# Performance work log

Measured on AMD Instinct MI355X. Metric: run time of the kernel, lower is better.

## Reference

```python
import jax, jax.numpy as jnp
import numpy as np

N_USERS, N_ITEMS, N_ENT = 2500, 3000, 2500
N = N_USERS + N_ITEMS + N_ENT
D, NREL, L, K, NH = 128, 32, 2, 16, 2
NE = 256_000
F_MOVIE, F_USER = 768, 512
GATE_T = 0.5


def _lin(x, w, b):
    return x @ w + b


def setup_inputs() -> dict:
    key = jax.random.key(0)
    ks = iter(jax.random.split(key, 64))
    def rn(shape, s=0.05):
        return jax.random.normal(next(ks), shape, jnp.float32) * s
    def zb():
        return jnp.zeros((D,), jnp.float32)
    inp = dict(
        user_w=rn((N_USERS, D), 0.1), item_w=rn((N_ITEMS, D), 0.1),
        ent_w=rn((N_ENT, D), 0.1), rel_w=rn((NREL, D), 0.1),
        mfeat=rn((N_ITEMS, F_MOVIE), 1.0), ufeat=rn((N_USERS, F_USER), 1.0),
        me_w1=rn((F_MOVIE, D)), me_b1=zb(), me_w2=rn((D, D)), me_b2=zb(),
        ue_w1=rn((F_USER, D)), ue_b1=zb(), ue_w2=rn((D, D)), ue_b2=zb(),
        cm_qw=rn((D, D)), cm_qb=zb(), cm_kw=rn((D, D)), cm_kb=zb(),
        cm_vw=rn((D, D)), cm_vb=zb(), cm_ow=rn((D, D)), cm_ob=zb(),
        mg_w=rn((2 * D, D)), mg_b=zb(), ug_w=rn((2 * D, D)), ug_b=zb(),
        gnn_qw=rn((L, D, D)), gnn_qb=jnp.zeros((L, D), jnp.float32),
        gnn_kw=rn((L, D, D)), gnn_kb=jnp.zeros((L, D), jnp.float32),
        gnn_vw=rn((L, D, D)), gnn_vb=jnp.zeros((L, D), jnp.float32),
        la_w=rn(((L + 1) * D, D)), la_b=zb(),
        adj_data=jax.random.uniform(next(ks), (NE,), jnp.float32, 1e-3, 1.0),
        adj_row=jax.random.randint(next(ks), (NE,), 0, N),
        adj_col=jax.random.randint(next(ks), (NE,), 0, N),
    )
    return inp


def _forward(user_w, item_w, ent_w, rel_w, mfeat, ufeat,
             me_w1, me_b1, me_w2, me_b2, ue_w1, ue_b1, ue_w2, ue_b2,
             cm_qw, cm_qb, cm_kw, cm_kb, cm_vw, cm_vb, cm_ow, cm_ob,
             mg_w, mg_b, ug_w, ug_b,
             gnn_qw, gnn_qb, gnn_kw, gnn_kb, gnn_vw, gnn_vb,
             la_w, la_b, adj_data, adj_row, adj_col):
    hd = D // NH
    # --- modality encoders (dropout is inference-mode identity) ---
    mm_item = jax.nn.relu(_lin(jax.nn.relu(_lin(mfeat, me_w1, me_b1)), me_w2, me_b2))
    mm_user = jax.nn.relu(_lin(jax.nn.relu(_lin(ufeat, ue_w1, ue_b1)), ue_w2, ue_b2))
    # --- MultiHeadCrossModalAttention(mm_item, mm_item): 2 modalities ---
    x = jnp.stack([mm_item, mm_item], axis=1)                     # [B, 2, D]
    B, M = x.shape[0], x.shape[1]
    q = _lin(x, cm_qw, cm_qb).reshape(B, M, NH, hd).transpose(0, 2, 1, 3)
    k = _lin(x, cm_kw, cm_kb).reshape(B, M, NH, hd).transpose(0, 2, 1, 3)
    v = _lin(x, cm_vw, cm_vb).reshape(B, M, NH, hd).transpose(0, 2, 1, 3)
    attn = jax.nn.softmax(jnp.einsum('bhmd,bhnd->bhmn', q, k) / jnp.sqrt(jnp.float32(hd)), axis=-1)
    ao = jnp.einsum('bhmn,bhnd->bhmd', attn, v).transpose(0, 2, 1, 3).reshape(B, M, D)
    mm_item = _lin(ao, cm_ow, cm_ob).sum(axis=1)                  # [B, D]
    # --- gated fusion (NOTE: double sigmoid, faithful to source) ---
    mg = jax.nn.sigmoid(jax.nn.sigmoid(_lin(jnp.concatenate([item_w, mm_item], axis=-1), mg_w, mg_b)) / GATE_T)
    fused_item = mg * item_w + (1.0 - mg) * mm_item + 0.1 * item_w
    ug = jax.nn.sigmoid(jax.nn.sigmoid(_lin(jnp.concatenate([user_w, mm_user], axis=-1), ug_w, ug_b)) / GATE_T)
    fused_user = ug * user_w + (1.0 - ug) * mm_user + 0.1 * user_w
    # --- GNN propagation with SparseKnowledgeAttention ---
    emb = jnp.concatenate([fused_user, fused_item, ent_w], axis=0)  # [N, D]
    rel_mean = rel_w.mean(axis=0)                                  # [D]
    embs = [emb]
    for l in range(L):
        e = embs[-1]
        # sparse adj @ e via gather + segment_sum
        side = jax.ops.segment_sum(adj_data[:, None] * e[adj_col], adj_row, num_segments=N)
        qn = _lin(e, gnn_qw[l], gnn_qb[l])
        kn = _lin(side * rel_mean[None, :], gnn_kw[l], gnn_kb[l])
        scores = (qn @ kn.T) / jnp.sqrt(jnp.float32(D))            # [N, N]
        tv, ti = jax.lax.top_k(scores, K)                          # [N, K]
        w = jax.nn.softmax(tv, axis=-1)
        vn = _lin(side, gnn_vw[l], gnn_vb[l])
        agg = jnp.einsum('nk,nkd->nd', w, vn[ti])                  # gather + weighted sum
        embs.append(jax.nn.relu(agg))
    final = _lin(jnp.concatenate(embs, axis=-1), la_w, la_b)       # layer_agg on stacked layers
    def _norm(z):
        return z / jnp.maximum(jnp.linalg.norm(z, axis=1, keepdims=True), 1e-12)
    return (_norm(final[:N_USERS]),
            _norm(final[N_USERS:N_USERS + N_ITEMS]),
            item_w, mm_item)


def reference(user_w, item_w, ent_w, rel_w, mfeat, ufeat,
              me_w1, me_b1, me_w2, me_b2, ue_w1, ue_b1, ue_w2, ue_b2,
              cm_qw, cm_qb, cm_kw, cm_kb, cm_vw, cm_vb, cm_ow, cm_ob,
              mg_w, mg_b, ug_w, ug_b,
              gnn_qw, gnn_qb, gnn_kw, gnn_kb, gnn_vw, gnn_vb,
              la_w, la_b, adj_data, adj_row, adj_col):
    return _forward(user_w, item_w, ent_w, rel_w, mfeat, ufeat,
                    me_w1, me_b1, me_w2, me_b2, ue_w1, ue_b1, ue_w2, ue_b2,
                    cm_qw, cm_qb, cm_kw, cm_kb, cm_vw, cm_vb, cm_ow, cm_ob,
                    mg_w, mg_b, ug_w, ug_b,
                    gnn_qw, gnn_qb, gnn_kw, gnn_kb, gnn_vw, gnn_vb,
                    la_w, la_b, adj_data, adj_row, adj_col)
```

## Files before the change

kernel.cpp:

```cpp
#include <hip/hip_runtime.h>
#include <hip/hip_bf16.h>
#include <math.h>

#define N_USERS 2500
#define N_ITEMS 3000
#define N_ENT   2500
#define NTOT    8000
#define D       128
#define NEDGE   256000
#define NSLICE  8
#define NMAT    12

typedef unsigned short u16;
typedef unsigned int u32;
typedef unsigned long long u64;
typedef __attribute__((ext_vector_type(8))) short short8;
typedef __attribute__((ext_vector_type(4))) float f32x4;

static __device__ __forceinline__ u16 bf16bits(float x) {
  __hip_bfloat16 h = __float2bfloat16(x);
  return *reinterpret_cast<u16*>(&h);
}

struct WsplitArgs {
  const float* w[NMAT];
  int useks[NMAT];
  int K[NMAT];
  int cum[NMAT + 1];
  int ofs[NMAT];
};

__global__ void k_wsplit_all(WsplitArgs a, const float* __restrict__ relmean,
                             u16* __restrict__ arena) {
  const int e = blockIdx.x * 256 + threadIdx.x;
  if (e >= a.cum[NMAT]) return;
  int i = 0;
  while (e >= a.cum[i + 1]) ++i;
  const int local = e - a.cum[i];
  const int k = local >> 7, j = local & 127;
  const int K = a.K[i];
  float x = a.w[i][(size_t)k * 128 + j];
  if (a.useks[i]) x *= relmean[k];
  const __hip_bfloat16 h1 = __float2bfloat16(x);
  const float r1 = x - __bfloat162float(h1);
  const __hip_bfloat16 h2 = __float2bfloat16(r1);
  const float r2 = r1 - __bfloat162float(h2);
  const __hip_bfloat16 h3 = __float2bfloat16(r2);
  u16* __restrict__ base = arena + a.ofs[i] + (size_t)j * K + k;
  base[0]                 = *(const u16*)&h1;
  base[(size_t)128 * K]   = *(const u16*)&h2;
  base[(size_t)256 * K * 1 + (size_t)0] = base[(size_t)256 * K];
  base[(size_t)256 * K]   = *(const u16*)&h3;
}

__global__ __launch_bounds__(256) void k_gemm3(const float* __restrict__ A,
                                               const u16* __restrict__ wsg,
                                               const float* __restrict__ b,
                                               float* __restrict__ out,
                                               u16* __restrict__ ob,
                                               int M, int K, int mode) {
  const int tid  = threadIdx.x;
  const int lane = tid & 63;
  const int wave = tid >> 6;
  const int rbase = blockIdx.x * 64 + wave * 16;
  const int colL = lane & 15;
  const int kofs = (lane >> 4) * 8;

  f32x4 acc[8];
#pragma unroll
  for (int ct = 0; ct < 8; ++ct) acc[ct] = (f32x4){0.f, 0.f, 0.f, 0.f};

  const int arow = (rbase + colL < M) ? (rbase + colL) : (M - 1);
  const float* __restrict__ arp = A + (size_t)arow * K;

  for (int k0 = 0; k0 < K; k0 += 32) {
    const float4 f0 = *(const float4*)(arp + k0 + kofs);
    const float4 f1 = *(const float4*)(arp + k0 + kofs + 4);
    float av[8] = {f0.x, f0.y, f0.z, f0.w, f1.x, f1.y, f1.z, f1.w};
    short8 a1, a2, a3;
#pragma unroll
    for (int e = 0; e < 8; ++e) {
      const float x = av[e];
      const __hip_bfloat16 h1 = __float2bfloat16(x);
      const float r1 = x - __bfloat162float(h1);
      const __hip_bfloat16 h2 = __float2bfloat16(r1);
      const float r2 = r1 - __bfloat162float(h2);
      const __hip_bfloat16 h3 = __float2bfloat16(r2);
      a1[e] = *(const short*)&h1;
      a2[e] = *(const short*)&h2;
      a3[e] = *(const short*)&h3;
    }
#pragma unroll
    for (int ct = 0; ct < 8; ++ct) {
      const int j = ct * 16 + colL;
      const u16* wp = wsg + (size_t)j * K + k0 + kofs;
      const short8 b1 = *(const short8*)wp;
      const short8 b2 = *(const short8*)(wp + (size_t)128 * K);
      const short8 b3 = *(const short8*)(wp + (size_t)256 * K);
      acc[ct] = __builtin_amdgcn_mfma_f32_16x16x32_bf16(a1, b1, acc[ct], 0, 0, 0);
      acc[ct] = __builtin_amdgcn_mfma_f32_16x16x32_bf16(a1, b2, acc[ct], 0, 0, 0);
      acc[ct] = __builtin_amdgcn_mfma_f32_16x16x32_bf16(a2, b1, acc[ct], 0, 0, 0);
      acc[ct] = __builtin_amdgcn_mfma_f32_16x16x32_bf16(a2, b2, acc[ct], 0, 0, 0);
      acc[ct] = __builtin_amdgcn_mfma_f32_16x16x32_bf16(a1, b3, acc[ct], 0, 0, 0);
      acc[ct] = __builtin_amdgcn_mfma_f32_16x16x32_bf16(a3, b1, acc[ct], 0, 0, 0);
    }
  }

#pragma unroll
  for (int ct = 0; ct < 8; ++ct) {
    const int j = ct * 16 + colL;
    const float bj = b[j];
#pragma unroll
    for (int r = 0; r < 4; ++r) {
      const int row = rbase + (lane >> 4) * 4 + r;
      if (row < M) {
        float c = acc[ct][r] + bj;
        if (mode == 1) c = fmaxf(c, 0.f);
        else if (mode == 2) c *= 2.f;
        out[(size_t)row * 128 + j] = c;
        if (ob) ob[(size_t)row * 128 + j] = bf16bits(c);
      }
    }
  }
}

__global__ __launch_bounds__(256) void k_gemm3x2(const float* __restrict__ A,
                                                 const u16* __restrict__ wsgA,
                                                 const float* __restrict__ bA,
                                                 float* __restrict__ outA,
                                                 u16* __restrict__ obA,
                                                 const u16* __restrict__ wsgB,
                                                 const float* __restrict__ bB,
                                                 float* __restrict__ outB,
                                                 int M, int K) {
  const int tid  = threadIdx.x;
  const int lane = tid & 63;
  const int wave = tid >> 6;
  const int rbase = blockIdx.x * 64 + wave * 16;
  const int colL = lane & 15;
  const int kofs = (lane >> 4) * 8;

  f32x4 accA[8], accB[8];
#pragma unroll
  for (int ct = 0; ct < 8; ++ct) {
    accA[ct] = (f32x4){0.f, 0.f, 0.f, 0.f};
    accB[ct] = (f32x4){0.f, 0.f, 0.f, 0.f};
  }

  const int arow = (rbase + colL < M) ? (rbase + colL) : (M - 1);
  const float* __restrict__ arp = A + (size_t)arow * K;

  for (int k0 = 0; k0 < K; k0 += 32) {
    const float4 f0 = *(const float4*)(arp + k0 + kofs);
    const float4 f1 = *(const float4*)(arp + k0 + kofs + 4);
    float av[8] = {f0.x, f0.y, f0.z, f0.w, f1.x, f1.y, f1.z, f1.w};
    short8 a1, a2, a3;
#pragma unroll
    for (int e = 0; e < 8; ++e) {
      const float x = av[e];
      const __hip_bfloat16 h1 = __float2bfloat16(x);
      const float r1 = x - __bfloat162float(h1);
      const __hip_bfloat16 h2 = __float2bfloat16(r1);
      const float r2 = r1 - __bfloat162float(h2);
      const __hip_bfloat16 h3 = __float2bfloat16(r2);
      a1[e] = *(const short*)&h1;
      a2[e] = *(const short*)&h2;
      a3[e] = *(const short*)&h3;
    }
#pragma unroll
    for (int ct = 0; ct < 8; ++ct) {
      const int j = ct * 16 + colL;
      {
        const u16* wp = wsgA + (size_t)j * K + k0 + kofs;
        const short8 b1 = *(const short8*)wp;
        const short8 b2 = *(const short8*)(wp + (size_t)128 * K);
        const short8 b3 = *(const short8*)(wp + (size_t)256 * K);
        accA[ct] = __builtin_amdgcn_mfma_f32_16x16x32_bf16(a1, b1, accA[ct], 0, 0, 0);
        accA[ct] = __builtin_amdgcn_mfma_f32_16x16x32_bf16(a1, b2, accA[ct], 0, 0, 0);
        accA[ct] = __builtin_amdgcn_mfma_f32_16x16x32_bf16(a2, b1, accA[ct], 0, 0, 0);
        accA[ct] = __builtin_amdgcn_mfma_f32_16x16x32_bf16(a2, b2, accA[ct], 0, 0, 0);
        accA[ct] = __builtin_amdgcn_mfma_f32_16x16x32_bf16(a1, b3, accA[ct], 0, 0, 0);
        accA[ct] = __builtin_amdgcn_mfma_f32_16x16x32_bf16(a3, b1, accA[ct], 0, 0, 0);
      }
      {
        const u16* wp = wsgB + (size_t)j * K + k0 + kofs;
        const short8 b1 = *(const short8*)wp;
        const short8 b2 = *(const short8*)(wp + (size_t)128 * K);
        const short8 b3 = *(const short8*)(wp + (size_t)256 * K);
        accB[ct] = __builtin_amdgcn_mfma_f32_16x16x32_bf16(a1, b1, accB[ct], 0, 0, 0);
        accB[ct] = __builtin_amdgcn_mfma_f32_16x16x32_bf16(a1, b2, accB[ct], 0, 0, 0);
        accB[ct] = __builtin_amdgcn_mfma_f32_16x16x32_bf16(a2, b1, accB[ct], 0, 0, 0);
        accB[ct] = __builtin_amdgcn_mfma_f32_16x16x32_bf16(a2, b2, accB[ct], 0, 0, 0);
        accB[ct] = __builtin_amdgcn_mfma_f32_16x16x32_bf16(a1, b3, accB[ct], 0, 0, 0);
        accB[ct] = __builtin_amdgcn_mfma_f32_16x16x32_bf16(a3, b1, accB[ct], 0, 0, 0);
      }
    }
  }

#pragma unroll
  for (int ct = 0; ct < 8; ++ct) {
    const int j = ct * 16 + colL;
    const float bjA = bA[j];
    const float bjB = bB[j];
#pragma unroll
    for (int r = 0; r < 4; ++r) {
      const int row = rbase + (lane >> 4) * 4 + r;
      if (row < M) {
        const float cA = accA[ct][r] + bjA;
        outA[(size_t)row * 128 + j] = cA;
        obA[(size_t)row * 128 + j] = bf16bits(cA);
        outB[(size_t)row * 128 + j] = accB[ct][r] + bjB;
      }
    }
  }
}

__global__ void k_gatefuse(const float* __restrict__ base, const float* __restrict__ mm,
                           const float* __restrict__ gw, const float* __restrict__ gb,
                           float* __restrict__ embout) {
  const int r = blockIdx.x;
  const int j = threadIdx.x;
  const float* __restrict__ b0 = base + (size_t)r * D;
  const float* __restrict__ m0 = mm + (size_t)r * D;
  float acc = 0.f;
  for (int k = 0; k < D; ++k) acc = fmaf(b0[k], gw[(size_t)k * D + j], acc);
  for (int k = 0; k < D; ++k) acc = fmaf(m0[k], gw[(size_t)(D + k) * D + j], acc);
  acc += gb[j];
  const float s1 = 1.f / (1.f + expf(-acc));
  const float g  = 1.f / (1.f + expf(-(s1 * 2.f)));
  const float bv = b0[j], mv = m0[j];
  embout[(size_t)r * D + j] = g * bv + (1.f - g) * mv + 0.1f * bv;
}

__global__ void k_relmean(const float* __restrict__ rel, float* __restrict__ out) {
  const int j = threadIdx.x;
  float s = 0.f;
  for (int i = 0; i < 32; ++i) s += rel[i * D + j];
  out[j] = s * (1.f / 32.f);
}

__global__ void k_copy3(const float* __restrict__ ent, const float* __restrict__ item,
                        const float* __restrict__ mm, float* __restrict__ emb0ent,
                        float* __restrict__ outItem, float* __restrict__ outMM) {
  const int t = blockIdx.x * 256 + threadIdx.x;
  const int nEnt = N_ENT * D;
  const int nIt  = N_ITEMS * D;
  if (t < nEnt) emb0ent[t] = ent[t];
  if (t < nIt) {
    outItem[t] = item[t];
    outMM[t]   = mm[t];
  }
}

__global__ void k_hist(const int* __restrict__ rw, int* __restrict__ cnt) {
  const int e = blockIdx.x * 256 + threadIdx.x;
  if (e < NEDGE) atomicAdd(&cnt[rw[e]], 1);
}

__global__ __launch_bounds__(1024) void k_scan(int* __restrict__ cnt,
                                               int* __restrict__ rowptr,
                                               int* __restrict__ cursor) {
  __shared__ int part[1024];
  const int t = threadIdx.x;
  const int base = t * 8;
  int loc[8];
  int s = 0;
#pragma unroll
  for (int j = 0; j < 8; ++j) {
    const int v = (base + j < NTOT) ? cnt[base + j] : 0;
    loc[j] = s; s += v;
  }
  part[t] = s;
  __syncthreads();
  for (int off = 1; off < 1024; off <<= 1) {
    const int v = (t >= off) ? part[t - off] : 0;
    __syncthreads();
    part[t] += v;
    __syncthreads();
  }
  const int pre = (t == 0) ? 0 : part[t - 1];
#pragma unroll
  for (int j = 0; j < 8; ++j) {
    if (base + j < NTOT) {
      const int p = pre + loc[j];
      rowptr[base + j] = p;
      cursor[base + j] = p;
    }
  }
  if (t == 1023) rowptr[NTOT] = part[1023];
}

__global__ void k_scatter(const int* __restrict__ rw, int* __restrict__ cursor,
                          int* __restrict__ perm) {
  const int e = blockIdx.x * 256 + threadIdx.x;
  if (e >= NEDGE) return;
  const int pos = atomicAdd(&cursor[rw[e]], 1);
  perm[pos] = e;
}

__global__ __launch_bounds__(128) void k_spmm_csr(const float* __restrict__ dat,
                                                  const int* __restrict__ cl,
                                                  const int* __restrict__ perm,
                                                  const int* __restrict__ rowptr,
                                                  const float* __restrict__ emb,
                                                  float* __restrict__ side) {
  const int r = blockIdx.x;
  const int d = threadIdx.x;
  const int beg = rowptr[r], end = rowptr[r + 1];
  float acc = 0.f;
  for (int i = beg; i < end; ++i) {
    const int ei = perm[i];
    acc = fmaf(dat[ei], emb[(size_t)cl[ei] * D + d], acc);
  }
  side[(size_t)r * D + d] = acc;
}

__global__ __launch_bounds__(256) void k_topk6v(const u16* __restrict__ qb,
                                                const u16* __restrict__ kb,
                                                int* __restrict__ cand) {
  __shared__ u64 km[4][8][97];
  const int tid  = threadIdx.x;
  const int lane = tid & 63;
  const int wave = tid >> 6;
  const int rbase = blockIdx.x * 16;
  const int sl   = blockIdx.y * 4 + wave;
  const int colL = lane & 15;
  const int g    = lane >> 4;
  const int kofs = g * 8;

  short8 aF[4];
  {
    const u16* ap = qb + (size_t)(rbase + colL) * D + kofs;
#pragma unroll
    for (int t = 0; t < 4; ++t) aF[t] = *reinterpret_cast<const short8*>(ap + t * 32);
  }

  float s[4][6]; int c[4][6];
#pragma unroll
  for (int r = 0; r < 4; ++r)
#pragma unroll
    for (int j = 0; j < 6; ++j) { s[r][j] = -3.0e38f; c[r][j] = 0x40000000 + colL * 6 + j; }

  const int tile0  = sl * 62 + (sl < 4 ? sl : 4);
  const int ntiles = 62 + (sl < 4 ? 1 : 0);
  const u16* bb = kb + (size_t)(tile0 * 16 + colL) * D + kofs;

  short8 bF[4];
#pragma unroll
  for (int t = 0; t < 4; ++t) bF[t] = *reinterpret_cast<const short8*>(bb + t * 32);

  for (int ct = 0; ct < ntiles; ++ct) {
    const int cn = (ct + 1 < ntiles) ? ct + 1 : ct;
    const u16* nb = bb + (size_t)cn * 16 * D;
    short8 bN[4];
#pragma unroll
    for (int t = 0; t < 4; ++t) bN[t] = *reinterpret_cast<const short8*>(nb + t * 32);

    f32x4 acc = {0.f, 0.f, 0.f, 0.f};
#pragma unroll
    for (int t = 0; t < 4; ++t)
      acc = __builtin_amdgcn_mfma_f32_16x16x32_bf16(aF[t], bF[t], acc, 0, 0, 0);

    const int colIdx = (tile0 + ct) * 16 + colL;
#pragma unroll
    for (int r = 0; r < 4; ++r) {
      float ks = acc[r]; int kc = colIdx;
      if (ks > s[r][5]) {
#pragma unroll
        for (int i = 0; i < 6; ++i) {
          const bool bgt = ks > s[r][i];
          const float os = s[r][i]; const int oc = c[r][i];
          s[r][i] = bgt ? ks : os;  c[r][i] = bgt ? kc : oc;
          ks      = bgt ? os : ks;  kc      = bgt ? oc : kc;
        }
      }
    }

#pragma unroll
    for (int t = 0; t < 4; ++t) bF[t] = bN[t];
  }

  u64 kk[4][6];
#pragma unroll
  for (int r = 0; r < 4; ++r)
#pragma unroll
    for (int j = 0; j < 6; ++j) {
      const u32 b = __builtin_bit_cast(u32, s[r][j]);
      const u32 mono = b ^ ((u32)(((int)b) >> 31) | 0x80000000u);
      kk[r][j] = ((u64)mono << 32) | (u64)(0xFFFFFFFFu - (u32)c[r][j]);
    }

  if (g < 2) {
#pragma unroll
    for (int r = 0; r < 4; ++r)
#pragma unroll
      for (int j = 0; j < 6; ++j)
        km[wave][4 * g + r][colL * 6 + j] = kk[r][j];
  }
  __syncthreads();
  if (g < 2) {
#pragma unroll
    for (int r = 0; r < 4; ++r) {
      int cnt[6] = {0, 0, 0, 0, 0, 0};
      for (int q2 = 0; q2 < 96; ++q2) {
        const u64 o = km[wave][4 * g + r][q2];
#pragma unroll
        for (int j = 0; j < 6; ++j) cnt[j] += (o > kk[r][j]) ? 1 : 0;
      }
      const int row = rbase + 4 * g + r;
#pragma unroll
      for (int j = 0; j < 6; ++j)
        if (cnt[j] < 16)
          cand[(size_t)row * 128 + sl * 16 + cnt[j]] = c[r][j];
    }
  }
  __syncthreads();
  if (g >= 2) {
#pragma unroll
    for (int r = 0; r < 4; ++r)
#pragma unroll
      for (int j = 0; j < 6; ++j)
        km[wave][4 * (g - 2) + r][colL * 6 + j] = kk[r][j];
  }
  __syncthreads();
  if (g >= 2) {
#pragma unroll
    for (int r = 0; r < 4; ++r) {
      int cnt[6] = {0, 0, 0, 0, 0, 0};
      for (int q2 = 0; q2 < 96; ++q2) {
        const u64 o = km[wave][4 * (g - 2) + r][q2];
#pragma unroll
        for (int j = 0; j < 6; ++j) cnt[j] += (o > kk[r][j]) ? 1 : 0;
      }
      const int row = rbase + 4 * g + r;
#pragma unroll
      for (int j = 0; j < 6; ++j)
        if (cnt[j] < 16)
          cand[(size_t)row * 128 + sl * 16 + cnt[j]] = c[r][j];
    }
  }
}

__global__ __launch_bounds__(64) void k_rescore128(const float* __restrict__ qn,
                                                   const float* __restrict__ kn,
                                                   const float* __restrict__ vn,
                                                   const int* __restrict__ cand,
                                                   float* __restrict__ enext) {
  const int row = blockIdx.x;
  const int lane = threadIdx.x;
  const int* cr = cand + (size_t)row * 128;
  const int c0 = cr[lane];
  const int c1 = cr[64 + lane];

  const float4* __restrict__ q4  = (const float4*)(qn + (size_t)row * D);
  const float4* __restrict__ k40 = (const float4*)(kn + (size_t)c0 * D);
  const float4* __restrict__ k41 = (const float4*)(kn + (size_t)c1 * D);
  float s0 = 0.f, s1 = 0.f;
#pragma unroll 8
  for (int j = 0; j < 32; ++j) {
    const float4 qv = q4[j];
    const float4 a = k40[j], b = k41[j];
    s0 = fmaf(qv.x, a.x, s0); s0 = fmaf(qv.y, a.y, s0);
    s0 = fmaf(qv.z, a.z, s0); s0 = fmaf(qv.w, a.w, s0);
    s1 = fmaf(qv.x, b.x, s1); s1 = fmaf(qv.y, b.y, s1);
    s1 = fmaf(qv.z, b.z, s1); s1 = fmaf(qv.w, b.w, s1);
  }
  const float inv = 0.088388347648318447f;
  s0 *= inv; s1 *= inv;

  int r0 = 0, r1 = 0;
  for (int j = 0; j < 64; ++j) {
    const float t0 = __shfl(s0, j), t1 = __shfl(s1, j);
    const int   u0 = __shfl(c0, j), u1 = __shfl(c1, j);
    r0 += (t0 > s0 || (t0 == s0 && u0 < c0)) ? 1 : 0;
    r0 += (t1 > s0 || (t1 == s0 && u1 < c0)) ? 1 : 0;
    r1 += (t0 > s1 || (t0 == s1 && u0 < c1)) ? 1 : 0;
    r1 += (t1 > s1 || (t1 == s1 && u1 < c1)) ? 1 : 0;
  }
  const bool sel0 = r0 < 16, sel1 = r1 < 16;

  float v = fmaxf(sel0 ? s0 : -3.0e38f, sel1 ? s1 : -3.0e38f);
#pragma unroll
  for (int d2 = 1; d2 < 64; d2 <<= 1) v = fmaxf(v, __shfl_xor(v, d2));
  const float e0 = sel0 ? expf(s0 - v) : 0.f;
  const float e1 = sel1 ? expf(s1 - v) : 0.f;
  float Z = e0 + e1;
#pragma unroll
  for (int d2 = 1; d2 < 64; d2 <<= 1) Z += __shfl_xor(Z, d2);
  const float w0 = e0 / Z, w1 = e1 / Z;

  float a0 = 0.f, a1 = 0.f;
  unsigned long long b0 = __ballot(sel0);
  while (b0) {
    const int src = __ffsll(b0) - 1; b0 &= b0 - 1;
    const float wj = __shfl(w0, src);
    const int   cj = __shfl(c0, src);
    const float* __restrict__ vr = vn + (size_t)cj * D;
    a0 = fmaf(wj, vr[lane], a0);
    a1 = fmaf(wj, vr[64 + lane], a1);
  }
  unsigned long long b1 = __ballot(sel1);
  while (b1) {
    const int src = __ffsll(b1) - 1; b1 &= b1 - 1;
    const float wj = __shfl(w1, src);
    const int   cj = __shfl(c1, src);
    const float* __restrict__ vr = vn + (size_t)cj * D;
    a0 = fmaf(wj, vr[lane], a0);
    a1 = fmaf(wj, vr[64 + lane], a1);
  }
  enext[(size_t)row * D + lane]      = fmaxf(a0, 0.f);
  enext[(size_t)row * D + 64 + lane] = fmaxf(a1, 0.f);
}

__global__ void k_final_norm(const float* __restrict__ e0, const float* __restrict__ e1,
                             const float* __restrict__ e2, const float* __restrict__ law,
                             const float* __restrict__ lab, float* __restrict__ out) {
  __shared__ float red[128];
  const int r = blockIdx.x;
  const int j = threadIdx.x;
  const float* __restrict__ a0 = e0 + (size_t)r * D;
  const float* __restrict__ a1 = e1 + (size_t)r * D;
  const float* __restrict__ a2 = e2 + (size_t)r * D;
  float acc = lab[j];
  for (int k = 0; k < D; ++k) acc = fmaf(a0[k], law[(size_t)k * D + j], acc);
  for (int k = 0; k < D; ++k) acc = fmaf(a1[k], law[(size_t)(D + k) * D + j], acc);
  for (int k = 0; k < D; ++k) acc = fmaf(a2[k], law[(size_t)(2 * D + k) * D + j], acc);
  red[j] = acc * acc;
  __syncthreads();
  for (int st = 64; st > 0; st >>= 1) {
    if (j < st) red[j] += red[j + st];
    __syncthreads();
  }
  const float nrm = fmaxf(sqrtf(red[0]), 1e-12f);
  const float o = acc / nrm;
  if (r < N_USERS) out[(size_t)r * D + j] = o;
  else             out[(size_t)N_USERS * D + (size_t)(r - N_USERS) * D + j] = o;
}

extern "C" void kernel_launch(void* const* d_in, const int* in_sizes, int n_in,
                              void* d_out, int out_size, void* d_ws, size_t ws_size,
                              hipStream_t stream) {
  const float* user_w = (const float*)d_in[0];
  const float* item_w = (const float*)d_in[1];
  const float* ent_w  = (const float*)d_in[2];
  const float* rel_w  = (const float*)d_in[3];
  const float* mfeat  = (const float*)d_in[4];
  const float* ufeat  = (const float*)d_in[5];
  const float* me_w1  = (const float*)d_in[6];
  const float* me_b1  = (const float*)d_in[7];
  const float* me_w2  = (const float*)d_in[8];
  const float* me_b2  = (const float*)d_in[9];
  const float* ue_w1  = (const float*)d_in[10];
  const float* ue_b1  = (const float*)d_in[11];
  const float* ue_w2  = (const float*)d_in[12];
  const float* ue_b2  = (const float*)d_in[13];
  const float* cm_vw  = (const float*)d_in[18];
  const float* cm_vb  = (const float*)d_in[19];
  const float* cm_ow  = (const float*)d_in[20];
  const float* cm_ob  = (const float*)d_in[21];
  const float* mg_w   = (const float*)d_in[22];
  const float* mg_b   = (const float*)d_in[23];
  const float* ug_w   = (const float*)d_in[24];
  const float* ug_b   = (const float*)d_in[25];
  const float* gnn_qw = (const float*)d_in[26];
  const float* gnn_qb = (const float*)d_in[27];
  const float* gnn_kw = (const float*)d_in[28];
  const float* gnn_kb = (const float*)d_in[29];
  const float* gnn_vw = (const float*)d_in[30];
  const float* gnn_vb = (const float*)d_in[31];
  const float* la_w   = (const float*)d_in[32];
  const float* la_b   = (const float*)d_in[33];
  const float* adj_d  = (const float*)d_in[34];
  const int*   adj_r  = (const int*)d_in[35];
  const int*   adj_c  = (const int*)d_in[36];
  float* out = (float*)d_out;
  float* ws  = (float*)d_ws;

  size_t off = 0;
  float* mm_item = ws + off; off += (size_t)N_ITEMS * D;
  float* mm_user = ws + off; off += (size_t)N_USERS * D;
  float* enc     = ws + off; off += (size_t)N_ITEMS * D;
  float* tmp     = ws + off; off += (size_t)N_ITEMS * D;
  float* emb0    = ws + off; off += (size_t)NTOT * D;
  float* emb1    = ws + off; off += (size_t)NTOT * D;
  float* emb2    = ws + off; off += (size_t)NTOT * D;
  float* side    = ws + off; off += (size_t)NTOT * D;
  float* qn      = ws + off; off += (size_t)NTOT * D;
  float* kn      = ws + off; off += (size_t)NTOT * D;
  float* vn      = ws + off; off += (size_t)NTOT * D;
  float* relmean = ws + off; off += D;
  u16* arena = (u16*)(ws + off); off += 491520;
  u16* qb = (u16*)mm_user;
  u16* kb = qb + (size_t)NTOT * D;
  int* cand = (int*)side;
  int* rowptr = (int*)emb2;
  int* cursor = rowptr + 8064;
  int* permB  = cursor + 8064;

  static const int Ks[NMAT]  = {768, 128, 512, 128, 128, 128, 128, 128, 128, 128, 128, 128};
  int ofs[NMAT], cum[NMAT + 1];
  {
    int o = 0, cc = 0;
    for (int i = 0; i < NMAT; ++i) {
      ofs[i] = o; o += 3 * Ks[i] * 128;
      cum[i] = cc; cc += Ks[i] * 128;
    }
    cum[NMAT] = cc;
  }

  WsplitArgs wa;
  const float* wptr[NMAT] = {me_w1, me_w2, ue_w1, ue_w2, cm_vw, cm_ow,
                             gnn_qw, gnn_kw, gnn_vw,
                             gnn_qw + (size_t)D * D, gnn_kw + (size_t)D * D,
                             gnn_vw + (size_t)D * D};
  for (int i = 0; i < NMAT; ++i) {
    wa.w[i] = wptr[i];
    wa.useks[i] = (i == 7 || i == 10) ? 1 : 0;
    wa.K[i] = Ks[i];
    wa.cum[i] = cum[i];
    wa.ofs[i] = ofs[i];
  }
  wa.cum[NMAT] = cum[NMAT];

  k_relmean<<<1, D, 0, stream>>>(rel_w, relmean);
  k_wsplit_all<<<(cum[NMAT] + 255) / 256, 256, 0, stream>>>(wa, relmean, arena);

  k_gemm3<<<(3000 + 63) / 64, 256, 0, stream>>>(mfeat, arena + ofs[0], me_b1, tmp, nullptr, 3000, 768, 1);
  k_gemm3<<<(3000 + 63) / 64, 256, 0, stream>>>(tmp, arena + ofs[1], me_b2, enc, nullptr, 3000, 128, 1);
  k_gemm3<<<(2500 + 63) / 64, 256, 0, stream>>>(ufeat, arena + ofs[2], ue_b1, tmp, nullptr, 2500, 512, 1);
  k_gemm3<<<(2500 + 63) / 64, 256, 0, stream>>>(tmp, arena + ofs[3], ue_b2, mm_user, nullptr, 2500, 128, 1);
  k_gemm3<<<(3000 + 63) / 64, 256, 0, stream>>>(enc, arena + ofs[4], cm_vb, tmp, nullptr, 3000, 128, 0);
  k_gemm3<<<(3000 + 63) / 64, 256, 0, stream>>>(tmp, arena + ofs[5], cm_ob, mm_item, nullptr, 3000, 128, 2);
  k_gatefuse<<<N_ITEMS, D, 0, stream>>>(item_w, mm_item, mg_w, mg_b, emb0 + (size_t)N_USERS * D);
  k_gatefuse<<<N_USERS, D, 0, stream>>>(user_w, mm_user, ug_w, ug_b, emb0);
  k_copy3<<<(N_ITEMS * D + 255) / 256, 256, 0, stream>>>(
      ent_w, item_w, mm_item,
      emb0 + (size_t)(N_USERS + N_ITEMS) * D,
      out + (size_t)(N_USERS + N_ITEMS) * D,
      out + (size_t)(N_USERS + 2 * N_ITEMS) * D);

  hipMemsetAsync(cursor, 0, NTOT * sizeof(int), stream);
  k_hist<<<(NEDGE + 255) / 256, 256, 0, stream>>>(adj_r, cursor);
  k_scan<<<1, 1024, 0, stream>>>(cursor, rowptr, cursor);
  k_scatter<<<(NEDGE + 255) / 256, 256, 0, stream>>>(adj_r, cursor, permB);

  const float* eml[3] = {emb0, emb1, emb2};
  for (int l = 0; l < 2; ++l) {
    const float* e = eml[l];
    float* enext   = (float*)eml[l + 1];
    k_spmm_csr<<<NTOT, 128, 0, stream>>>(adj_d, adj_c, permB, rowptr, e, side);
    k_gemm3<<<(NTOT + 63) / 64, 256, 0, stream>>>(e, arena + ofs[6 + 3 * l],
                                                  gnn_qb + (size_t)l * D, qn, qb, NTOT, 128, 0);
    k_gemm3x2<<<(NTOT + 63) / 64, 256, 0, stream>>>(side,
                                                    arena + ofs[7 + 3 * l], gnn_kb + (size_t)l * D, kn, kb,
                                                    arena + ofs[8 + 3 * l], gnn_vb + (size_t)l * D, vn,
                                                    NTOT, 128);
    dim3 tkgrid(NTOT / 16, 2);
    k_topk6v<<<tkgrid, 256, 0, stream>>>(qb, kb, cand);
    k_rescore128<<<NTOT, 64, 0, stream>>>(qn, kn, vn, cand, enext);
  }

  k_final_norm<<<N_USERS + N_ITEMS, D, 0, stream>>>(emb0, emb1, emb2, la_w, la_b, out);
}
```

Measured before the change: 1.143 ms.

## Split each top-k key slice across two waves and merge partial top-16 lists

The top-k candidate kernel now gives each key slice its own block of two waves. The waves take alternating 16-column tiles, so each wave does half the MFMA and insertion work per slice, and the grid grows from 2 to 8 slices in y. Each wave's per-row top-16 is staged in shared memory, and a rank-count merge of the two sorted lists writes the final 16 candidates. It also drops a redundant self-copy store in the weight-split kernel. In exchange it adds extra syncs, a merge step, and duplicated loading of the A fragments per block.

```diff
diff --git a/kernel.cpp b/kernel.cpp
--- a/kernel.cpp
+++ b/kernel.cpp
@@ -47,10 +47,9 @@
   const float r2 = r1 - __bfloat162float(h2);
   const __hip_bfloat16 h3 = __float2bfloat16(r2);
   u16* __restrict__ base = arena + a.ofs[i] + (size_t)j * K + k;
-  base[0]                 = *(const u16*)&h1;
-  base[(size_t)128 * K]   = *(const u16*)&h2;
-  base[(size_t)256 * K * 1 + (size_t)0] = base[(size_t)256 * K];
-  base[(size_t)256 * K]   = *(const u16*)&h3;
+  base[0]               = *(const u16*)&h1;
+  base[(size_t)128 * K] = *(const u16*)&h2;
+  base[(size_t)256 * K] = *(const u16*)&h3;
 }
 
 __global__ __launch_bounds__(256) void k_gemm3(const float* __restrict__ A,
@@ -315,15 +314,17 @@
   side[(size_t)r * D + d] = acc;
 }
 
-__global__ __launch_bounds__(256) void k_topk6v(const u16* __restrict__ qb,
+__global__ __launch_bounds__(128) void k_topk6p(const u16* __restrict__ qb,
                                                 const u16* __restrict__ kb,
                                                 int* __restrict__ cand) {
-  __shared__ u64 km[4][8][97];
+  __shared__ u64 km[8][97];
+  __shared__ u64 k2[2][16][17];
+  __shared__ int c2[2][16][17];
   const int tid  = threadIdx.x;
   const int lane = tid & 63;
   const int wave = tid >> 6;
   const int rbase = blockIdx.x * 16;
-  const int sl   = blockIdx.y * 4 + wave;
+  const int sl   = blockIdx.y;
   const int colL = lane & 15;
   const int g    = lane >> 4;
   const int kofs = g * 8;
@@ -345,12 +346,14 @@
   const int ntiles = 62 + (sl < 4 ? 1 : 0);
   const u16* bb = kb + (size_t)(tile0 * 16 + colL) * D + kofs;
 
+  int ct = wave;
   short8 bF[4];
 #pragma unroll
-  for (int t = 0; t < 4; ++t) bF[t] = *reinterpret_cast<const short8*>(bb + t * 32);
-
-  for (int ct = 0; ct < ntiles; ++ct) {
-    const int cn = (ct + 1 < ntiles) ? ct + 1 : ct;
+  for (int t = 0; t < 4; ++t)
+    bF[t] = *reinterpret_cast<const short8*>(bb + (size_t)ct * 16 * D + t * 32);
+
+  for (; ct < ntiles; ct += 2) {
+    const int cn = (ct + 2 < ntiles) ? ct + 2 : ct;
     const u16* nb = bb + (size_t)cn * 16 * D;
     short8 bN[4];
 #pragma unroll
@@ -390,53 +393,55 @@
       kk[r][j] = ((u64)mono << 32) | (u64)(0xFFFFFFFFu - (u32)c[r][j]);
     }
 
-  if (g < 2) {
-#pragma unroll
-    for (int r = 0; r < 4; ++r)
-#pragma unroll
-      for (int j = 0; j < 6; ++j)
-        km[wave][4 * g + r][colL * 6 + j] = kk[r][j];
-  }
-  __syncthreads();
-  if (g < 2) {
-#pragma unroll
-    for (int r = 0; r < 4; ++r) {
-      int cnt[6] = {0, 0, 0, 0, 0, 0};
-      for (int q2 = 0; q2 < 96; ++q2) {
-        const u64 o = km[wave][4 * g + r][q2];
-#pragma unroll
-        for (int j = 0; j < 6; ++j) cnt[j] += (o > kk[r][j]) ? 1 : 0;
+  for (int p = 0; p < 2; ++p) {
+    for (int h = 0; h < 2; ++h) {
+      const bool act = (wave == p) && ((g >> 1) == h);
+      if (act) {
+#pragma unroll
+        for (int r = 0; r < 4; ++r)
+#pragma unroll
+          for (int j = 0; j < 6; ++j)
+            km[4 * (g & 1) + r][colL * 6 + j] = kk[r][j];
       }
-      const int row = rbase + 4 * g + r;
-#pragma unroll
-      for (int j = 0; j < 6; ++j)
-        if (cnt[j] < 16)
-          cand[(size_t)row * 128 + sl * 16 + cnt[j]] = c[r][j];
-    }
-  }
-  __syncthreads();
-  if (g >= 2) {
-#pragma unroll
-    for (int r = 0; r < 4; ++r)
-#pragma unroll
-      for (int j = 0; j < 6; ++j)
-        km[wave][4 * (g - 2) + r][colL * 6 + j] = kk[r][j];
-  }
-  __syncthreads();
-  if (g >= 2) {
-#pragma unroll
-    for (int r = 0; r < 4; ++r) {
-      int cnt[6] = {0, 0, 0, 0, 0, 0};
-      for (int q2 = 0; q2 < 96; ++q2) {
-        const u64 o = km[wave][4 * (g - 2) + r][q2];
-#pragma unroll
-        for (int j = 0; j < 6; ++j) cnt[j] += (o > kk[r][j]) ? 1 : 0;
+      __syncthreads();
+      if (act) {
+#pragma unroll
+        for (int r = 0; r < 4; ++r) {
+          const int row8 = 4 * (g & 1) + r;
+          int cnt[6] = {0, 0, 0, 0, 0, 0};
+#pragma unroll 8
+          for (int q2 = 0; q2 < 96; ++q2) {
+            const u64 o = km[row8][q2];
+#pragma unroll
+            for (int j = 0; j < 6; ++j) cnt[j] += (o > kk[r][j]) ? 1 : 0;
+          }
+          const int row = 4 * g + r;
+#pragma unroll
+          for (int j = 0; j < 6; ++j)
+            if (cnt[j] < 16) {
+              k2[p][row][cnt[j]] = kk[r][j];
+              c2[p][row][cnt[j]] = c[r][j];
+            }
+        }
       }
-      const int row = rbase + 4 * g + r;
-#pragma unroll
-      for (int j = 0; j < 6; ++j)
-        if (cnt[j] < 16)
-          cand[(size_t)row * 128 + sl * 16 + cnt[j]] = c[r][j];
+      __syncthreads();
+    }
+  }
+
+  {
+    const int row = lane >> 2;
+    const int q0 = (lane & 3) * 4;
+#pragma unroll
+    for (int qq = 0; qq < 4; ++qq) {
+      const int q = q0 + qq;
+      const u64 key = k2[wave][row][q];
+      int cnt1 = 0;
+#pragma unroll
+      for (int q2 = 0; q2 < 16; ++q2)
+        cnt1 += (k2[1 - wave][row][q2] > key) ? 1 : 0;
+      const int slot = q + cnt1;
+      if (slot < 16)
+        cand[(size_t)(rbase + row) * 128 + sl * 16 + slot] = c2[wave][row][q];
     }
   }
 }
@@ -655,8 +660,8 @@
                                                     arena + ofs[7 + 3 * l], gnn_kb + (size_t)l * D, kn, kb,
                                                     arena + ofs[8 + 3 * l], gnn_vb + (size_t)l * D, vn,
                                                     NTOT, 128);
-    dim3 tkgrid(NTOT / 16, 2);
-    k_topk6v<<<tkgrid, 256, 0, stream>>>(qb, kb, cand);
+    dim3 tkgrid(NTOT / 16, NSLICE);
+    k_topk6p<<<tkgrid, 128, 0, stream>>>(qb, kb, cand);
     k_rescore128<<<NTOT, 64, 0, stream>>>(qn, kn, vn, cand, enext);
   }
 
```

Measured after the change: 1.370 ms. 19.8% more time.
